# Kernel tuning notes

Hardware: AMD Instinct MI355X
Metric: run time of the kernel (lower is better)

The kernel has to match this reference:

```python
import jax, jax.numpy as jnp
import numpy as np

WOW1 = 121  # first ring-padding window
WOW2 = 5    # second ring-padding window


def ring_windows(x, wow):
    """Circular sliding windows: [B, L, C] -> [B, L, wow*C].
    Window i covers original indices (i - (wow-1) + j) mod L, j=0..wow-1,
    matching torch cat([x[:, -wow+1:], x], 1) followed by unfold+stack."""
    B, L, C = x.shape
    idx = (jnp.arange(L)[:, None] + jnp.arange(wow)[None, :] - (wow - 1)) % L  # [L, wow]
    return x[:, idx, :].reshape(B, L, wow * C)


def _linear_params(key, fan_in, fan_out):
    k1, k2 = jax.random.split(key)
    s = 1.0 / np.sqrt(fan_in)
    W = jax.random.uniform(k1, (fan_in, fan_out), minval=-s, maxval=s, dtype=jnp.float32)
    b = jax.random.uniform(k2, (fan_out,), minval=-s, maxval=s, dtype=jnp.float32)
    return W, b


def setup_inputs() -> dict:
    key = jax.random.key(0)
    ks = jax.random.split(key, 7)
    B, L, C = 8, 4096, 4
    sps, nos = 128, 32
    x = jax.random.normal(ks[0], (B, L, C), dtype=jnp.float32)
    W0, b0 = _linear_params(ks[1], WOW1 * C, sps // 4)       # 484 -> 32
    W1, b1 = _linear_params(ks[2], sps // 4, 4 * sps)        # 32 -> 512
    Ws, bs = _linear_params(ks[3], 4 * sps, nos * sps)       # 512 -> 4096 (shared_dense_0)
    Wr, br = _linear_params(ks[4], nos * sps, 4)             # 4096 -> 4 (reshape_layer)
    W2, b2 = _linear_params(ks[5], WOW2 * 4, 8 * 4)          # 20 -> 32
    W3, b3 = _linear_params(ks[6], 8 * 4, 4)                 # 32 -> 4
    return {"x": x, "W0": W0, "b0": b0, "W1": W1, "b1": b1,
            "Ws": Ws, "bs": bs, "Wr": Wr, "br": br,
            "W2": W2, "b2": b2, "W3": W3, "b3": b3}


def reference(x, W0, b0, W1, b1, Ws, bs, Wr, br, W2, b2, W3, b3):
    h = ring_windows(x, WOW1)                 # [B, L, 484]
    h = jnp.tanh(h @ W0 + b0)                 # [B, L, sps//4]
    h = h @ W1 + b1                           # [B, L, 4*sps]
    h = h @ Ws + bs                           # [B, L, nos*sps]
    h = h @ Wr + br                           # [B, L, 4]
    h = ring_windows(h, WOW2)                 # [B, L, 20]
    h = jax.nn.relu(h @ W2 + b2)              # [B, L, 32]
    return h @ W3 + b3                        # [B, L, 4]
```

## Files before the change

### kernel.cpp

```cpp
#include <hip/hip_runtime.h>
#include <hip/hip_bf16.h>
#include <math.h>


#define L_SEQ 4096

typedef __attribute__((ext_vector_type(8))) short  bf16x8;
typedef __attribute__((ext_vector_type(4))) float  f32x4;

static __device__ __forceinline__ unsigned short f2bf(float f) {
  union { float f; unsigned int u; } v; v.f = f;
  unsigned int u = v.u + 0x7fffu + ((v.u >> 16) & 1u);
  return (unsigned short)(u >> 16);
}

__global__ __launch_bounds__(256) void precomp1_kernel(
    const float* __restrict__ Ws, const float* __restrict__ bs,
    const float* __restrict__ Wr, float* __restrict__ T) {
  const int tid  = threadIdx.x;
  const int k    = blockIdx.x * 4 + (tid >> 6);
  const int lane = tid & 63;
  if (k >= 513) return;
  const float4* row4 = (const float4*)((k < 512) ? (Ws + (size_t)k * 4096) : bs);
  const float4* Wr4  = (const float4*)Wr;
  float a0 = 0.f, a1 = 0.f, a2 = 0.f, a3 = 0.f;
#pragma unroll 4
  for (int m4 = lane; m4 < 1024; m4 += 64) {
    const float4 rv = row4[m4];
#pragma unroll
    for (int c = 0; c < 4; ++c) {
      const float  xs = ((const float*)&rv)[c];
      const float4 w  = Wr4[m4 * 4 + c];
      a0 = fmaf(xs, w.x, a0); a1 = fmaf(xs, w.y, a1);
      a2 = fmaf(xs, w.z, a2); a3 = fmaf(xs, w.w, a3);
    }
  }
#pragma unroll
  for (int off = 32; off > 0; off >>= 1) {
    a0 += __shfl_xor(a0, off); a1 += __shfl_xor(a1, off);
    a2 += __shfl_xor(a2, off); a3 += __shfl_xor(a3, off);
  }
  if (lane == 0) {
    float4 o; o.x = a0; o.y = a1; o.z = a2; o.w = a3;
    ((float4*)T)[k] = o;
  }
}

__global__ __launch_bounds__(128) void precomp2_kernel(
    const float* __restrict__ W1, const float* __restrict__ b1,
    const float* __restrict__ br, const float* __restrict__ T,
    float* __restrict__ WcBc) {
  const int i   = blockIdx.x;
  const int t   = threadIdx.x;
  const int j   = t & 3;
  const int seg = t >> 2;
  const float4* v4 = (const float4*)((i < 32) ? (W1 + (size_t)i * 512) : b1);
  const float4* T4 = (const float4*)T;
  float acc = 0.f;
#pragma unroll
  for (int q = 0; q < 4; ++q) {
    const int m4 = seg * 4 + q;
    const float4 vv = v4[m4];
#pragma unroll
    for (int c = 0; c < 4; ++c) {
      const float4 trow = T4[m4 * 4 + c];
      acc = fmaf(((const float*)&vv)[c], ((const float*)&trow)[j], acc);
    }
  }
  __shared__ float red[128];
  red[t] = acc;
  __syncthreads();
#pragma unroll
  for (int s = 64; s >= 4; s >>= 1) {
    if (t < s) red[t] += red[t + s];
    __syncthreads();
  }
  if (t < 4) {
    float r = red[t];
    if (i == 32) r += T[512 * 4 + t] + br[t];
    WcBc[(i < 32 ? i * 4 : 128) + t] = r;
  }
}

__global__ __launch_bounds__(256) void precompW_kernel(
    const float* __restrict__ W0, unsigned short* __restrict__ Bfrag) {
  const int t  = blockIdx.x * 256 + threadIdx.x;
  const int f  = t >> 6;
  const int l  = t & 63;
  const int kk = f >> 1;
  const int nh = f & 1;
  const int n  = nh * 16 + (l & 15);
  unsigned int pk[4];
#pragma unroll
  for (int p = 0; p < 4; ++p) {
    const int k0 = kk * 32 + (l >> 4) * 8 + p * 2;
    const float v0 = (k0     < 484) ? W0[(size_t)k0 * 32 + n]       : 0.f;
    const float v1 = (k0 + 1 < 484) ? W0[(size_t)(k0 + 1) * 32 + n] : 0.f;
    pk[p] = (unsigned int)f2bf(v0) | ((unsigned int)f2bf(v1) << 16);
  }
  uint4 o; o.x = pk[0]; o.y = pk[1]; o.z = pk[2]; o.w = pk[3];
  ((uint4*)Bfrag)[t] = o;
}

__global__ __launch_bounds__(256) void stage1_kernel(
    const float* __restrict__ x, const unsigned short* __restrict__ Bfrag,
    const float* __restrict__ b0, const float* __restrict__ WcBc,
    float* __restrict__ y) {
  __shared__ unsigned short sX[192 * 4];
  __shared__ float sH[64][33];
  __shared__ float sWc[132];

  const int b    = blockIdx.x >> 6;
  const int tile = blockIdx.x & 63;
  const int l0   = tile * 64;
  const int tid  = threadIdx.x;

  if (tid < 192) {
    float4 v = {0.f, 0.f, 0.f, 0.f};
    if (tid < 184)
      v = ((const float4*)(x + (size_t)b * L_SEQ * 4))[(l0 - 120 + tid) & (L_SEQ - 1)];
    ushort4 u;
    u.x = f2bf(v.x); u.y = f2bf(v.y); u.z = f2bf(v.z); u.w = f2bf(v.w);
    *(ushort4*)(sX + tid * 4) = u;
  }
  if (tid < 132) sWc[tid] = WcBc[tid];
  __syncthreads();

  const int lane = tid & 63;
  const int wid  = tid >> 6;
  const int rowb = wid * 16;

  const bf16x8* Bf = (const bf16x8*)Bfrag;
  bf16x8 bw[32];
#pragma unroll
  for (int f = 0; f < 32; ++f) bw[f] = Bf[f * 64 + lane];

  const float bias0 = b0[lane & 15];
  const float bias1 = b0[16 + (lane & 15)];

  f32x4 acc0 = {0.f, 0.f, 0.f, 0.f};
  f32x4 acc1 = {0.f, 0.f, 0.f, 0.f};

#pragma unroll
  for (int kk = 0; kk < 16; ++kk) {
    const int p0 = rowb + (lane & 15) + kk * 8 + 2 * (lane >> 4);
    union { uint4 u; bf16x8 v; } af;
    const uint2 lo = *(const uint2*)(sX + p0 * 4);
    const uint2 hi = *(const uint2*)(sX + p0 * 4 + 4);
    af.u.x = lo.x; af.u.y = lo.y; af.u.z = hi.x; af.u.w = hi.y;
    acc0 = __builtin_amdgcn_mfma_f32_16x16x32_bf16(af.v, bw[kk * 2 + 0], acc0, 0, 0, 0);
    acc1 = __builtin_amdgcn_mfma_f32_16x16x32_bf16(af.v, bw[kk * 2 + 1], acc1, 0, 0, 0);
  }

#pragma unroll
  for (int r = 0; r < 4; ++r) {
    const int row = rowb + (lane >> 4) * 4 + r;
    const float s0 = acc0[r] + bias0;
    const float s1 = acc1[r] + bias1;
    sH[row][lane & 15]      = 1.f - 2.f / (__expf(2.f * s0) + 1.f);
    sH[row][16 + (lane & 15)] = 1.f - 2.f / (__expf(2.f * s1) + 1.f);
  }
  __syncthreads();

  {
    const int rr = tid >> 2;
    const int j  = tid & 3;
    float o = sWc[128 + j];
#pragma unroll
    for (int n = 0; n < 32; ++n) o = fmaf(sH[rr][n], sWc[n * 4 + j], o);
    y[((size_t)b * L_SEQ + l0 + rr) * 4 + j] = o;
  }
}

__global__ __launch_bounds__(128) void stage2_kernel(
    const float* __restrict__ y, const float* __restrict__ W2,
    const float* __restrict__ b2, const float* __restrict__ W3,
    const float* __restrict__ b3, float* __restrict__ out) {
  const int g = blockIdx.x * 128 + threadIdx.x;
  const int b = g >> 12;
  const int l = g & (L_SEQ - 1);
  const float4* yv = (const float4*)(y + (size_t)b * L_SEQ * 4);

  float win[20];
#pragma unroll
  for (int j = 0; j < 5; ++j) {
    const float4 v = yv[(l - 4 + j) & (L_SEQ - 1)];
    win[j*4+0] = v.x; win[j*4+1] = v.y; win[j*4+2] = v.z; win[j*4+3] = v.w;
  }

  float h[32];
#pragma unroll
  for (int n = 0; n < 32; ++n) h[n] = b2[n];
#pragma unroll
  for (int k = 0; k < 20; ++k) {
    const float xs = win[k];
#pragma unroll
    for (int n = 0; n < 32; ++n) h[n] = fmaf(xs, W2[k*32 + n], h[n]);
  }

  float o[4];
#pragma unroll
  for (int j = 0; j < 4; ++j) o[j] = b3[j];
#pragma unroll
  for (int n = 0; n < 32; ++n) {
    const float hv = fmaxf(h[n], 0.f);
#pragma unroll
    for (int j = 0; j < 4; ++j) o[j] = fmaf(hv, W3[n*4 + j], o[j]);
  }
  float4 ov;
  ((float*)&ov)[0] = o[0]; ((float*)&ov)[1] = o[1];
  ((float*)&ov)[2] = o[2]; ((float*)&ov)[3] = o[3];
  ((float4*)out)[g] = ov;
}

extern "C" void kernel_launch(void* const* d_in, const int* in_sizes, int n_in,
                              void* d_out, int out_size, void* d_ws, size_t ws_size,
                              hipStream_t stream) {
  const float* x  = (const float*)d_in[0];
  const float* W0 = (const float*)d_in[1];
  const float* b0 = (const float*)d_in[2];
  const float* W1 = (const float*)d_in[3];
  const float* b1 = (const float*)d_in[4];
  const float* Ws = (const float*)d_in[5];
  const float* bs = (const float*)d_in[6];
  const float* Wr = (const float*)d_in[7];
  const float* br = (const float*)d_in[8];
  const float* W2 = (const float*)d_in[9];
  const float* b2 = (const float*)d_in[10];
  const float* W3 = (const float*)d_in[11];
  const float* b3 = (const float*)d_in[12];
  float* outp = (float*)d_out;

  float* T    = (float*)d_ws;
  float* WcBc = T + 2052;
  float* y    = (float*)d_ws + 2304;
  unsigned short* Bfrag = (unsigned short*)((float*)d_ws + 133376);

  precomp1_kernel<<<129, 256, 0, stream>>>(Ws, bs, Wr, T);
  precomp2_kernel<<<33, 128, 0, stream>>>(W1, b1, br, T, WcBc);
  precompW_kernel<<<8, 256, 0, stream>>>(W0, Bfrag);
  stage1_kernel<<<512, 256, 0, stream>>>(x, Bfrag, b0, WcBc, y);
  stage2_kernel<<<256, 128, 0, stream>>>(y, W2, b2, W3, b3, outp);
}
```

Before: 109.7 us.

## Fuse stage1 and stage2 with halo recompute and merge small precompute kernels

Merges the two small precompute kernels into one launch that splits work by block index. Fuses stage1 and stage2 into a single 320-thread kernel. Each 64-row tile recomputes 4 extra halo rows of the hidden projection so the 5-wide circular window can be read from shared memory. This removes the y round trip through global memory and two kernel launches, in exchange for about 6% redundant MFMA work and a fifth wave per block.

```diff
diff --git a/kernel.cpp b/kernel.cpp
--- a/kernel.cpp
+++ b/kernel.cpp
@@ -4,6 +4,7 @@
 
 
 #define L_SEQ 4096
+#define NPOS  208
 
 typedef __attribute__((ext_vector_type(8))) short  bf16x8;
 typedef __attribute__((ext_vector_type(4))) float  f32x4;
@@ -46,68 +47,73 @@
   }
 }
 
-__global__ __launch_bounds__(128) void precomp2_kernel(
+__global__ __launch_bounds__(256) void precomp_small_kernel(
     const float* __restrict__ W1, const float* __restrict__ b1,
     const float* __restrict__ br, const float* __restrict__ T,
-    float* __restrict__ WcBc) {
-  const int i   = blockIdx.x;
-  const int t   = threadIdx.x;
-  const int j   = t & 3;
-  const int seg = t >> 2;
-  const float4* v4 = (const float4*)((i < 32) ? (W1 + (size_t)i * 512) : b1);
-  const float4* T4 = (const float4*)T;
-  float acc = 0.f;
-#pragma unroll
-  for (int q = 0; q < 4; ++q) {
-    const int m4 = seg * 4 + q;
-    const float4 vv = v4[m4];
-#pragma unroll
-    for (int c = 0; c < 4; ++c) {
-      const float4 trow = T4[m4 * 4 + c];
-      acc = fmaf(((const float*)&vv)[c], ((const float*)&trow)[j], acc);
-    }
-  }
-  __shared__ float red[128];
-  red[t] = acc;
-  __syncthreads();
-#pragma unroll
-  for (int s = 64; s >= 4; s >>= 1) {
-    if (t < s) red[t] += red[t + s];
+    float* __restrict__ WcBc,
+    const float* __restrict__ W0, unsigned short* __restrict__ Bfrag) {
+  if (blockIdx.x < 33) {
+    const int i = blockIdx.x;
+    const int t = threadIdx.x;
+    __shared__ float red[128];
+    float acc = 0.f;
+    if (t < 128) {
+      const int j   = t & 3;
+      const int seg = t >> 2;
+      const float4* v4 = (const float4*)((i < 32) ? (W1 + (size_t)i * 512) : b1);
+      const float4* T4 = (const float4*)T;
+#pragma unroll
+      for (int q = 0; q < 4; ++q) {
+        const int m4 = seg * 4 + q;
+        const float4 vv = v4[m4];
+#pragma unroll
+        for (int c = 0; c < 4; ++c) {
+          const float4 trow = T4[m4 * 4 + c];
+          acc = fmaf(((const float*)&vv)[c], ((const float*)&trow)[j], acc);
+        }
+      }
+      red[t] = acc;
+    }
     __syncthreads();
-  }
-  if (t < 4) {
-    float r = red[t];
-    if (i == 32) r += T[512 * 4 + t] + br[t];
-    WcBc[(i < 32 ? i * 4 : 128) + t] = r;
-  }
-}
-
-__global__ __launch_bounds__(256) void precompW_kernel(
-    const float* __restrict__ W0, unsigned short* __restrict__ Bfrag) {
-  const int t  = blockIdx.x * 256 + threadIdx.x;
-  const int f  = t >> 6;
-  const int l  = t & 63;
-  const int kk = f >> 1;
-  const int nh = f & 1;
-  const int n  = nh * 16 + (l & 15);
-  unsigned int pk[4];
-#pragma unroll
-  for (int p = 0; p < 4; ++p) {
-    const int k0 = kk * 32 + (l >> 4) * 8 + p * 2;
-    const float v0 = (k0     < 484) ? W0[(size_t)k0 * 32 + n]       : 0.f;
-    const float v1 = (k0 + 1 < 484) ? W0[(size_t)(k0 + 1) * 32 + n] : 0.f;
-    pk[p] = (unsigned int)f2bf(v0) | ((unsigned int)f2bf(v1) << 16);
-  }
-  uint4 o; o.x = pk[0]; o.y = pk[1]; o.z = pk[2]; o.w = pk[3];
-  ((uint4*)Bfrag)[t] = o;
-}
-
-__global__ __launch_bounds__(256) void stage1_kernel(
+#pragma unroll
+    for (int s = 64; s >= 4; s >>= 1) {
+      if (t < s) red[t] += red[t + s];
+      __syncthreads();
+    }
+    if (t < 4) {
+      float r = red[t];
+      if (i == 32) r += T[512 * 4 + t] + br[t];
+      WcBc[(i < 32 ? i * 4 : 128) + t] = r;
+    }
+  } else {
+    const int t  = (blockIdx.x - 33) * 256 + threadIdx.x;
+    const int f  = t >> 6;
+    const int l  = t & 63;
+    const int kk = f >> 1;
+    const int nh = f & 1;
+    const int n  = nh * 16 + (l & 15);
+    unsigned int pk[4];
+#pragma unroll
+    for (int p = 0; p < 4; ++p) {
+      const int k0 = kk * 32 + (l >> 4) * 8 + p * 2;
+      const float v0 = (k0     < 484) ? W0[(size_t)k0 * 32 + n]       : 0.f;
+      const float v1 = (k0 + 1 < 484) ? W0[(size_t)(k0 + 1) * 32 + n] : 0.f;
+      pk[p] = (unsigned int)f2bf(v0) | ((unsigned int)f2bf(v1) << 16);
+    }
+    uint4 o; o.x = pk[0]; o.y = pk[1]; o.z = pk[2]; o.w = pk[3];
+    ((uint4*)Bfrag)[t] = o;
+  }
+}
+
+__global__ __launch_bounds__(320) void stage12_kernel(
     const float* __restrict__ x, const unsigned short* __restrict__ Bfrag,
     const float* __restrict__ b0, const float* __restrict__ WcBc,
-    float* __restrict__ y) {
-  __shared__ unsigned short sX[192 * 4];
-  __shared__ float sH[64][33];
+    const float* __restrict__ W2, const float* __restrict__ b2,
+    const float* __restrict__ W3, const float* __restrict__ b3,
+    float* __restrict__ out) {
+  __shared__ unsigned short sX[NPOS * 4];
+  __shared__ float sH[68][33];
+  __shared__ float sYv[68][4];
   __shared__ float sWc[132];
 
   const int b    = blockIdx.x >> 6;
@@ -115,10 +121,10 @@
   const int l0   = tile * 64;
   const int tid  = threadIdx.x;
 
-  if (tid < 192) {
+  if (tid < NPOS) {
     float4 v = {0.f, 0.f, 0.f, 0.f};
-    if (tid < 184)
-      v = ((const float4*)(x + (size_t)b * L_SEQ * 4))[(l0 - 120 + tid) & (L_SEQ - 1)];
+    if (tid < 188)
+      v = ((const float4*)(x + (size_t)b * L_SEQ * 4))[(l0 - 124 + tid) & (L_SEQ - 1)];
     ushort4 u;
     u.x = f2bf(v.x); u.y = f2bf(v.y); u.z = f2bf(v.z); u.w = f2bf(v.w);
     *(ushort4*)(sX + tid * 4) = u;
@@ -155,62 +161,49 @@
 #pragma unroll
   for (int r = 0; r < 4; ++r) {
     const int row = rowb + (lane >> 4) * 4 + r;
-    const float s0 = acc0[r] + bias0;
-    const float s1 = acc1[r] + bias1;
-    sH[row][lane & 15]      = 1.f - 2.f / (__expf(2.f * s0) + 1.f);
-    sH[row][16 + (lane & 15)] = 1.f - 2.f / (__expf(2.f * s1) + 1.f);
+    if (row < 68) {
+      const float s0 = acc0[r] + bias0;
+      const float s1 = acc1[r] + bias1;
+      sH[row][lane & 15]        = 1.f - 2.f / (__expf(2.f * s0) + 1.f);
+      sH[row][16 + (lane & 15)] = 1.f - 2.f / (__expf(2.f * s1) + 1.f);
+    }
   }
   __syncthreads();
 
-  {
+  if (tid < 272) {
     const int rr = tid >> 2;
     const int j  = tid & 3;
     float o = sWc[128 + j];
 #pragma unroll
     for (int n = 0; n < 32; ++n) o = fmaf(sH[rr][n], sWc[n * 4 + j], o);
-    y[((size_t)b * L_SEQ + l0 + rr) * 4 + j] = o;
-  }
-}
-
-__global__ __launch_bounds__(128) void stage2_kernel(
-    const float* __restrict__ y, const float* __restrict__ W2,
-    const float* __restrict__ b2, const float* __restrict__ W3,
-    const float* __restrict__ b3, float* __restrict__ out) {
-  const int g = blockIdx.x * 128 + threadIdx.x;
-  const int b = g >> 12;
-  const int l = g & (L_SEQ - 1);
-  const float4* yv = (const float4*)(y + (size_t)b * L_SEQ * 4);
-
-  float win[20];
-#pragma unroll
-  for (int j = 0; j < 5; ++j) {
-    const float4 v = yv[(l - 4 + j) & (L_SEQ - 1)];
-    win[j*4+0] = v.x; win[j*4+1] = v.y; win[j*4+2] = v.z; win[j*4+3] = v.w;
-  }
-
-  float h[32];
-#pragma unroll
-  for (int n = 0; n < 32; ++n) h[n] = b2[n];
-#pragma unroll
-  for (int k = 0; k < 20; ++k) {
-    const float xs = win[k];
-#pragma unroll
-    for (int n = 0; n < 32; ++n) h[n] = fmaf(xs, W2[k*32 + n], h[n]);
-  }
-
-  float o[4];
-#pragma unroll
-  for (int j = 0; j < 4; ++j) o[j] = b3[j];
-#pragma unroll
-  for (int n = 0; n < 32; ++n) {
-    const float hv = fmaxf(h[n], 0.f);
-#pragma unroll
-    for (int j = 0; j < 4; ++j) o[j] = fmaf(hv, W3[n*4 + j], o[j]);
-  }
-  float4 ov;
-  ((float*)&ov)[0] = o[0]; ((float*)&ov)[1] = o[1];
-  ((float*)&ov)[2] = o[2]; ((float*)&ov)[3] = o[3];
-  ((float4*)out)[g] = ov;
+    sYv[rr][j] = o;
+  }
+  __syncthreads();
+
+  if (tid < 256) {
+    const int rr = tid >> 2;
+    const int j  = tid & 3;
+    float win[20];
+#pragma unroll
+    for (int jj = 0; jj < 5; ++jj) {
+      const float4 v = *(const float4*)&sYv[rr + jj][0];
+      win[jj*4+0] = v.x; win[jj*4+1] = v.y; win[jj*4+2] = v.z; win[jj*4+3] = v.w;
+    }
+    float h[32];
+#pragma unroll
+    for (int n = 0; n < 32; ++n) h[n] = b2[n];
+#pragma unroll
+    for (int k = 0; k < 20; ++k) {
+      const float xs = win[k];
+#pragma unroll
+      for (int n = 0; n < 32; ++n) h[n] = fmaf(xs, W2[k*32 + n], h[n]);
+    }
+    float o = b3[j];
+#pragma unroll
+    for (int n = 0; n < 32; ++n)
+      o = fmaf(fmaxf(h[n], 0.f), W3[n*4 + j], o);
+    out[((size_t)b * L_SEQ + l0 + rr) * 4 + j] = o;
+  }
 }
 
 extern "C" void kernel_launch(void* const* d_in, const int* in_sizes, int n_in,
@@ -233,12 +226,9 @@
 
   float* T    = (float*)d_ws;
   float* WcBc = T + 2052;
-  float* y    = (float*)d_ws + 2304;
-  unsigned short* Bfrag = (unsigned short*)((float*)d_ws + 133376);
+  unsigned short* Bfrag = (unsigned short*)((float*)d_ws + 2304);
 
   precomp1_kernel<<<129, 256, 0, stream>>>(Ws, bs, Wr, T);
-  precomp2_kernel<<<33, 128, 0, stream>>>(W1, b1, br, T, WcBc);
-  precompW_kernel<<<8, 256, 0, stream>>>(W0, Bfrag);
-  stage1_kernel<<<512, 256, 0, stream>>>(x, Bfrag, b0, WcBc, y);
-  stage2_kernel<<<256, 128, 0, stream>>>(y, W2, b2, W3, b3, outp);
-}
+  precomp_small_kernel<<<41, 256, 0, stream>>>(W1, b1, br, T, WcBc, W0, Bfrag);
+  stage12_kernel<<<512, 320, 0, stream>>>(x, Bfrag, b0, WcBc, W2, b2, W3, b3, outp);
+}
```

After: 107.0 us. 1.03x faster.
